# Kernel tuning notes

Hardware: AMD Instinct MI355X
Metric: run time of the kernel (lower is better)

Reference implementation:

```python
import jax, jax.numpy as jnp
import numpy as np

N, D_IN, D_HID, D_OUT = 100000, 128, 512, 256
EPS = 1e-5


def _kaiming_uniform(k, shape):
    # torch kaiming_uniform_(a=sqrt(5)) -> bound = sqrt(1/fan_in)
    fan_in = shape[1]
    bound = float(np.sqrt(1.0 / fan_in))
    return jax.random.uniform(k, shape, minval=-bound, maxval=bound, dtype=jnp.float32)


def setup_inputs() -> dict:
    key = jax.random.key(0)
    ks = jax.random.split(key, 10)
    in_set = jax.random.normal(ks[0], (N, D_IN), dtype=jnp.float32)
    matA0 = _kaiming_uniform(ks[1], (D_HID, D_IN))
    matB0 = _kaiming_uniform(ks[2], (D_HID, D_IN))
    matA1 = _kaiming_uniform(ks[3], (D_HID, D_HID))
    matB1 = _kaiming_uniform(ks[4], (D_HID, D_HID))
    matA2 = _kaiming_uniform(ks[5], (D_HID, D_HID))
    matB2 = _kaiming_uniform(ks[6], (D_HID, D_HID))
    ln_gamma = jnp.ones((D_HID,), dtype=jnp.float32)
    ln_beta = jnp.zeros((D_HID,), dtype=jnp.float32)
    out_bound = float(np.sqrt(1.0 / D_HID))
    out_w = jax.random.uniform(ks[7], (D_OUT, D_HID), minval=-out_bound, maxval=out_bound, dtype=jnp.float32)
    out_b = jax.random.uniform(ks[8], (D_OUT,), minval=-out_bound, maxval=out_bound, dtype=jnp.float32)
    return {"in_set": in_set, "matA0": matA0, "matB0": matB0, "matA1": matA1, "matB1": matB1,
            "matA2": matA2, "matB2": matB2, "ln_gamma": ln_gamma, "ln_beta": ln_beta,
            "out_w": out_w, "out_b": out_b}


def _layer(h, A, B, g, b):
    # f(x_i) = relu(LN(A x_i + B (sum_j x_j - x_i)))
    # vectorized: h @ (A-B)^T + total_sum @ B^T  (sum-minus-self identity)
    s = h.sum(axis=0)  # [d]
    h = h @ (A - B).T + s @ B.T  # [N, d_hid]
    mu = h.mean(axis=-1, keepdims=True)
    var = jnp.mean((h - mu) ** 2, axis=-1, keepdims=True)
    h = (h - mu) / jnp.sqrt(var + EPS) * g + b
    return jax.nn.relu(h)


def reference(in_set, matA0, matB0, matA1, matB1, matA2, matB2, ln_gamma, ln_beta, out_w, out_b):
    h = _layer(in_set, matA0, matB0, ln_gamma, ln_beta)
    h = _layer(h, matA1, matB1, ln_gamma, ln_beta)
    h = _layer(h, matA2, matB2, ln_gamma, ln_beta)
    h = h.max(axis=0)  # max-pool over set elements -> [d_hid]
    return h @ out_w.T + out_b  # [d_out]
```

## Files before the change

kernel.cpp:

```cpp
#include <hip/hip_runtime.h>
#include <hip/hip_bf16.h>

#define NPTS 100000
#define NPTS_PAD 100096
#define DHID 512
#define EPSV 1e-5f

typedef __attribute__((ext_vector_type(4))) float f32x4;

#define OFF_INBF   0UL
#define OFF_W0     12812288UL
#define OFF_W1     12877824UL
#define OFF_W2     13139968UL
#define OFF_C0     13402112UL
#define OFF_C1     13404160UL
#define OFF_C2     13406208UL
#define OFF_PARTS  13408256UL
#define OFF_PARTS2 16609280UL
#define OFF_PARTS3 16740352UL
#define OFF_H1     16756736UL
#define OFF_H2     68005888UL

typedef const __attribute__((address_space(1))) unsigned int* gp_t;
typedef __attribute__((address_space(3))) unsigned int* lp_t;

__device__ __forceinline__ void async_copy16(const void* g, void* l) {
    __builtin_amdgcn_global_load_lds((gp_t)g, (lp_t)l, 16, 0, 0);
}

__device__ __forceinline__ unsigned pack4_fp8(float a, float b, float c, float d) {
    unsigned v = (unsigned)__builtin_amdgcn_cvt_pk_fp8_f32(a, b, 0, false);
    v = (unsigned)__builtin_amdgcn_cvt_pk_fp8_f32(c, d, (int)v, true);
    return v;
}

__global__ __launch_bounds__(256) void cvt_pack_kernel(const float* __restrict__ in,
                                                       unsigned char* __restrict__ out) {
    long total = (long)NPTS * 2;
    long stride = (long)gridDim.x * blockDim.x;
    for (long idx = (long)blockIdx.x * blockDim.x + threadIdx.x; idx < total; idx += stride) {
        int kt = (int)(idx / NPTS);
        long r = idx - (long)kt * NPTS;
        const float* src = in + r * 128 + kt * 64;
        unsigned dw[16];
#pragma unroll
        for (int j = 0; j < 16; ++j)
            dw[j] = pack4_fp8(src[4 * j], src[4 * j + 1], src[4 * j + 2], src[4 * j + 3]);
        uint4* dst = (uint4*)(out + ((long)kt * NPTS_PAD + r) * 64);
#pragma unroll
        for (int j = 0; j < 4; ++j)
            dst[j] = make_uint4(dw[4 * j], dw[4 * j + 1], dw[4 * j + 2], dw[4 * j + 3]);
    }
}

__global__ __launch_bounds__(256) void wpack_all_kernel(const float* __restrict__ A0,
                                                        const float* __restrict__ B0,
                                                        const float* __restrict__ A1,
                                                        const float* __restrict__ B1,
                                                        const float* __restrict__ A2,
                                                        const float* __restrict__ B2,
                                                        unsigned long long* __restrict__ W0,
                                                        unsigned long long* __restrict__ W1,
                                                        unsigned long long* __restrict__ W2) {
    int idx = blockIdx.x * 256 + threadIdx.x;
    const float *A, *B; unsigned long long* W; int KD, u;
    if (idx < 8192)       { A = A0; B = B0; W = W0; KD = 128; u = idx; }
    else if (idx < 40960) { A = A1; B = B1; W = W1; KD = 512; u = idx - 8192; }
    else                  { A = A2; B = B2; W = W2; KD = 512; u = idx - 40960; if (u >= 32768) return; }
    int F = (KD / 64) * 8;
    int lane = u & 63;
    int f = (u >> 6) % F;
    int wid = u / (64 * F);
    int ks = f >> 3, fn = (f >> 1) & 3, s = f & 1;
    int row = wid * 64 + fn * 16 + (lane & 15);
    int kb = ks * 64 + s * 32 + (lane >> 4) * 8;
    const float* sa = A + (long)row * KD + kb;
    const float* sb = B + (long)row * KD + kb;
    unsigned lo = pack4_fp8(sa[0] - sb[0], sa[1] - sb[1], sa[2] - sb[2], sa[3] - sb[3]);
    unsigned hi = pack4_fp8(sa[4] - sb[4], sa[5] - sb[5], sa[6] - sb[6], sa[7] - sb[7]);
    W[u] = ((unsigned long long)hi << 32) | lo;
}

__global__ __launch_bounds__(256) void colsum_in_kernel(const float* __restrict__ in,
                                                        float* __restrict__ parts) {
    __shared__ float sh[256];
    int t = threadIdx.x, blk = blockIdx.x;
    int c = t & 127, half = t >> 7;
    long rbeg = (long)blk * 196 + half;
    long rend = (long)(blk + 1) * 196; if (rend > NPTS) rend = NPTS;
    float s = 0.f;
    for (long r = rbeg; r < rend; r += 2) s += in[r * 128 + c];
    sh[t] = s;
    __syncthreads();
    if (t < 128) parts[blk * 128 + t] = sh[t] + sh[t + 128];
}

__global__ void part_reduceW_kernel(const float* __restrict__ parts, int nparts, int width,
                                    int op, float* __restrict__ out) {
    int g = blockIdx.x, t = threadIdx.x;
    int chunk = (nparts + gridDim.x - 1) / gridDim.x;
    int b0 = g * chunk, b1 = b0 + chunk; if (b1 > nparts) b1 = nparts;
    float s = 0.f;
    for (int b = b0; b < b1; ++b) {
        float v = parts[(long)b * width + t];
        s = (op == 0) ? (s + v) : fmaxf(s, v);
    }
    out[(long)g * width + t] = s;
}

__global__ __launch_bounds__(64) void gemv_fold_kernel(const float* __restrict__ p3, int dsum,
                                                       const float* __restrict__ Bm,
                                                       const float* __restrict__ bias, int op,
                                                       float* __restrict__ out) {
    int j = blockIdx.x, t = threadIdx.x;
    float acc = 0.f;
    for (int d = t; d < dsum; d += 64) {
        float s = 0.f;
#pragma unroll
        for (int g = 0; g < 8; ++g) {
            float v = p3[(long)g * dsum + d];
            s = (op == 0) ? (s + v) : fmaxf(s, v);
        }
        acc += s * Bm[(long)j * dsum + d];
    }
#pragma unroll
    for (int m = 32; m >= 1; m >>= 1) acc += __shfl_down(acc, m);
    if (t == 0) out[j] = acc + (bias ? bias[j] : 0.0f);
}

template<int KD, bool STORE, int REDOP>
__global__ __launch_bounds__(512, 4)
void layer_kernel(const unsigned char* __restrict__ Xp, const unsigned long long* __restrict__ Wp,
                  const float* __restrict__ cvec, const float* __restrict__ gvec,
                  const float* __restrict__ bvec, unsigned char* __restrict__ Hout,
                  float* __restrict__ red_out) {
    static_assert(KD % 64 == 0, "");
    constexpr int NK = KD / 64;
    __shared__ __align__(128) char smem[NK * 4096];

    const int t = threadIdx.x;
    const int lane = t & 63;
    const int wid = t >> 6;
    const int ln15 = lane & 15;
    const int lg = lane >> 4;
    const long row0 = (long)blockIdx.x * 64;

    f32x4 acc[4][4];
#pragma unroll
    for (int i = 0; i < 4; ++i)
#pragma unroll
        for (int j = 0; j < 4; ++j) acc[i][j] = (f32x4){0.f, 0.f, 0.f, 0.f};

    if (t < 256) {
        const int sr = t >> 2;
        const int ss = t & 3;
        const char* Xsrc = (const char*)Xp + (row0 + sr) * 64 + ((ss ^ ((sr >> 1) & 3)) * 16);
#pragma unroll
        for (int kt = 0; kt < NK; ++kt)
            async_copy16(Xsrc + (long)kt * (NPTS_PAD * 64), smem + kt * 4096 + t * 16);
    }
    __syncthreads();

#define RD8X(BASE, r, sub) (*(const long*)((BASE) + (r) * 64 + \
        (((((sub) * 2 + (lg >> 1)) ^ (((r) >> 1) & 3)) * 16) + (lg & 1) * 8)))

    const unsigned long long* Wq = Wp + (long)wid * (NK * 8) * 64 + lane;
#pragma unroll
    for (int ks = 0; ks < NK; ++ks) {
        const char* Xs = smem + ks * 4096;
        long a0[4], a1[4];
#pragma unroll
        for (int fm = 0; fm < 4; ++fm) {
            int r = fm * 16 + ln15;
            a0[fm] = RD8X(Xs, r, 0);
            a1[fm] = RD8X(Xs, r, 1);
        }
#pragma unroll
        for (int fn = 0; fn < 4; ++fn) {
            long w0 = (long)Wq[(ks * 8 + fn * 2 + 0) * 64];
            long w1 = (long)Wq[(ks * 8 + fn * 2 + 1) * 64];
#pragma unroll
            for (int fm = 0; fm < 4; ++fm)
                acc[fm][fn] = __builtin_amdgcn_mfma_f32_16x16x32_fp8_fp8(a0[fm], w0, acc[fm][fn], 0, 0, 0);
#pragma unroll
            for (int fm = 0; fm < 4; ++fm)
                acc[fm][fn] = __builtin_amdgcn_mfma_f32_16x16x32_fp8_fp8(a1[fm], w1, acc[fm][fn], 0, 0, 0);
        }
    }
#undef RD8X
    __syncthreads();

    float* lnred_s = (float*)smem;
    float* lnred_q = (float*)(smem + 2048);
    float* lnmv    = (float*)(smem + 4096);

    const int cbase = wid * 64 + ln15;
    float cv[4], gv[4], bv[4];
#pragma unroll
    for (int fn = 0; fn < 4; ++fn) {
        int col = cbase + fn * 16;
        cv[fn] = cvec[col]; gv[fn] = gvec[col]; bv[fn] = bvec[col];
    }

#pragma unroll
    for (int fm = 0; fm < 4; ++fm)
#pragma unroll
        for (int fn = 0; fn < 4; ++fn) acc[fm][fn] += cv[fn];

    float rs[16], rq[16];
#pragma unroll
    for (int fm = 0; fm < 4; ++fm)
#pragma unroll
        for (int j = 0; j < 4; ++j) {
            float s = 0.f, q = 0.f;
#pragma unroll
            for (int fn = 0; fn < 4; ++fn) {
                float x = acc[fm][fn][j];
                s += x; q += x * x;
            }
            rs[fm * 4 + j] = s; rq[fm * 4 + j] = q;
        }
#pragma unroll
    for (int m = 1; m < 16; m <<= 1)
#pragma unroll
        for (int i = 0; i < 16; ++i) {
            rs[i] += __shfl_xor(rs[i], m);
            rq[i] += __shfl_xor(rq[i], m);
        }
    if (ln15 == 0) {
#pragma unroll
        for (int fm = 0; fm < 4; ++fm)
#pragma unroll
            for (int j = 0; j < 4; ++j) {
                int row = fm * 16 + lg * 4 + j;
                lnred_s[row * 8 + wid] = rs[fm * 4 + j];
                lnred_q[row * 8 + wid] = rq[fm * 4 + j];
            }
    }
    __syncthreads();
    if (t < 64) {
        float s = 0.f, q = 0.f;
#pragma unroll
        for (int w = 0; w < 8; ++w) { s += lnred_s[t * 8 + w]; q += lnred_q[t * 8 + w]; }
        float mu = s * (1.0f / 512.0f);
        float var = q * (1.0f / 512.0f) - mu * mu;
        lnmv[t * 2] = mu;
        lnmv[t * 2 + 1] = rsqrtf(var + EPSV);
    }
    __syncthreads();

#pragma unroll
    for (int fm = 0; fm < 4; ++fm)
#pragma unroll
        for (int j = 0; j < 4; ++j) {
            int rloc = fm * 16 + lg * 4 + j;
            long rglob = row0 + rloc;
            bool ok = rglob < NPTS;
            float mu = lnmv[rloc * 2], rstd = lnmv[rloc * 2 + 1];
#pragma unroll
            for (int fn = 0; fn < 4; ++fn) {
                float y = fmaxf((acc[fm][fn][j] - mu) * rstd * gv[fn] + bv[fn], 0.0f);
                acc[fm][fn][j] = ok ? y : 0.0f;
            }
            if (STORE && ok) {
#pragma unroll
                for (int p = 0; p < 2; ++p) {
                    unsigned u = (unsigned)__builtin_amdgcn_cvt_pk_fp8_f32(
                        acc[fm][2 * p][j], acc[fm][2 * p + 1][j], 0, false);
                    Hout[((long)wid * NPTS_PAD + rglob) * 64 + (2 * p) * 16 + ln15] =
                        (unsigned char)(u & 0xff);
                    Hout[((long)wid * NPTS_PAD + rglob) * 64 + (2 * p + 1) * 16 + ln15] =
                        (unsigned char)((u >> 8) & 0xff);
                }
            }
        }

    float cp[4];
#pragma unroll
    for (int fn = 0; fn < 4; ++fn) {
        float p = 0.f;
#pragma unroll
        for (int fm = 0; fm < 4; ++fm)
#pragma unroll
            for (int j = 0; j < 4; ++j) {
                float v = acc[fm][fn][j];
                p = (REDOP == 0) ? (p + v) : fmaxf(p, v);
            }
        cp[fn] = p;
    }
#pragma unroll
    for (int m = 16; m < 64; m <<= 1)
#pragma unroll
        for (int fn = 0; fn < 4; ++fn) {
            float o = __shfl_xor(cp[fn], m);
            cp[fn] = (REDOP == 0) ? (cp[fn] + o) : fmaxf(cp[fn], o);
        }
    if (lane < 16) {
#pragma unroll
        for (int fn = 0; fn < 4; ++fn)
            red_out[(long)blockIdx.x * 512 + wid * 64 + fn * 16 + lane] = cp[fn];
    }
}

extern "C" void kernel_launch(void* const* d_in, const int* in_sizes, int n_in,
                              void* d_out, int out_size, void* d_ws, size_t ws_size,
                              hipStream_t stream) {
    const float* in_set = (const float*)d_in[0];
    const float* A0 = (const float*)d_in[1];
    const float* B0 = (const float*)d_in[2];
    const float* A1 = (const float*)d_in[3];
    const float* B1 = (const float*)d_in[4];
    const float* A2 = (const float*)d_in[5];
    const float* B2 = (const float*)d_in[6];
    const float* ga = (const float*)d_in[7];
    const float* be = (const float*)d_in[8];
    const float* ow = (const float*)d_in[9];
    const float* ob = (const float*)d_in[10];
    float* outp = (float*)d_out;
    char* ws = (char*)d_ws;

    unsigned char* in_f8 = (unsigned char*)(ws + OFF_INBF);
    unsigned long long* W0p = (unsigned long long*)(ws + OFF_W0);
    unsigned long long* W1p = (unsigned long long*)(ws + OFF_W1);
    unsigned long long* W2p = (unsigned long long*)(ws + OFF_W2);
    float* c0 = (float*)(ws + OFF_C0);
    float* c1 = (float*)(ws + OFF_C1);
    float* c2 = (float*)(ws + OFF_C2);
    float* parts = (float*)(ws + OFF_PARTS);
    float* parts2 = (float*)(ws + OFF_PARTS2);
    float* parts3 = (float*)(ws + OFF_PARTS3);
    unsigned char* h1 = (unsigned char*)(ws + OFF_H1);
    unsigned char* h2 = (unsigned char*)(ws + OFF_H2);

    const int nblk = (NPTS + 63) / 64;

    cvt_pack_kernel<<<1024, 256, 0, stream>>>(in_set, in_f8);
    wpack_all_kernel<<<288, 256, 0, stream>>>(A0, B0, A1, B1, A2, B2, W0p, W1p, W2p);

    colsum_in_kernel<<<512, 256, 0, stream>>>(in_set, parts);
    part_reduceW_kernel<<<64, 128, 0, stream>>>(parts, 512, 128, 0, parts2);
    part_reduceW_kernel<<<8, 128, 0, stream>>>(parts2, 64, 128, 0, parts3);
    gemv_fold_kernel<<<512, 64, 0, stream>>>(parts3, 128, B0, nullptr, 0, c0);

    layer_kernel<128, true, 0><<<nblk, 512, 0, stream>>>(in_f8, W0p, c0, ga, be, h1, parts);
    part_reduceW_kernel<<<64, 512, 0, stream>>>(parts, nblk, 512, 0, parts2);
    part_reduceW_kernel<<<8, 512, 0, stream>>>(parts2, 64, 512, 0, parts3);
    gemv_fold_kernel<<<512, 64, 0, stream>>>(parts3, 512, B1, nullptr, 0, c1);

    layer_kernel<512, true, 0><<<nblk, 512, 0, stream>>>(h1, W1p, c1, ga, be, h2, parts);
    part_reduceW_kernel<<<64, 512, 0, stream>>>(parts, nblk, 512, 0, parts2);
    part_reduceW_kernel<<<8, 512, 0, stream>>>(parts2, 64, 512, 0, parts3);
    gemv_fold_kernel<<<512, 64, 0, stream>>>(parts3, 512, B2, nullptr, 0, c2);

    layer_kernel<512, false, 1><<<nblk, 512, 0, stream>>>(h2, W2p, c2, ga, be, nullptr, parts);
    part_reduceW_kernel<<<64, 512, 0, stream>>>(parts, nblk, 512, 1, parts2);
    part_reduceW_kernel<<<8, 512, 0, stream>>>(parts2, 64, 512, 1, parts3);
    gemv_fold_kernel<<<256, 64, 0, stream>>>(parts3, 512, ow, ob, 1, outp);
}
```

Measured before the change: 309.5 us.

## Interleave fp8 K layout so hidden activations store as packed dwords

Changes the fp8 packed layout of the K dimension so that element k=16*m+c sits at byte 4*c+m inside each 64-byte row chunk. The input packer, weight packer and epilogue store all switch to this permuted layout consistently. The epilogue now writes one 32-bit word per row instead of four scattered byte stores, which cuts store instruction count and partial-write traffic. The row-bound check is dropped from the store, so padded rows also get written, which is safe only because the buffer is padded.

```diff
diff --git a/kernel.cpp b/kernel.cpp
--- a/kernel.cpp
+++ b/kernel.cpp
@@ -44,8 +44,8 @@
         const float* src = in + r * 128 + kt * 64;
         unsigned dw[16];
 #pragma unroll
-        for (int j = 0; j < 16; ++j)
-            dw[j] = pack4_fp8(src[4 * j], src[4 * j + 1], src[4 * j + 2], src[4 * j + 3]);
+        for (int m = 0; m < 16; ++m)
+            dw[m] = pack4_fp8(src[m], src[16 + m], src[32 + m], src[48 + m]);
         uint4* dst = (uint4*)(out + ((long)kt * NPTS_PAD + r) * 64);
 #pragma unroll
         for (int j = 0; j < 4; ++j)
@@ -72,12 +72,15 @@
     int f = (u >> 6) % F;
     int wid = u / (64 * F);
     int ks = f >> 3, fn = (f >> 1) & 3, s = f & 1;
-    int row = wid * 64 + fn * 16 + (lane & 15);
-    int kb = ks * 64 + s * 32 + (lane >> 4) * 8;
-    const float* sa = A + (long)row * KD + kb;
-    const float* sb = B + (long)row * KD + kb;
-    unsigned lo = pack4_fp8(sa[0] - sb[0], sa[1] - sb[1], sa[2] - sb[2], sa[3] - sb[3]);
-    unsigned hi = pack4_fp8(sa[4] - sb[4], sa[5] - sb[5], sa[6] - sb[6], sa[7] - sb[7]);
+    int ln15 = lane & 15, lg = lane >> 4;
+    int row = wid * 64 + fn * 16 + ln15;
+    int c0 = s * 8 + lg * 2;
+    const float* sa = A + (long)row * KD + ks * 64;
+    const float* sb = B + (long)row * KD + ks * 64;
+    unsigned lo = pack4_fp8(sa[c0] - sb[c0], sa[16 + c0] - sb[16 + c0],
+                            sa[32 + c0] - sb[32 + c0], sa[48 + c0] - sb[48 + c0]);
+    unsigned hi = pack4_fp8(sa[c0 + 1] - sb[c0 + 1], sa[17 + c0] - sb[17 + c0],
+                            sa[33 + c0] - sb[33 + c0], sa[49 + c0] - sb[49 + c0]);
     W[u] = ((unsigned long long)hi << 32) | lo;
 }
 
@@ -262,16 +265,9 @@
                 float y = fmaxf((acc[fm][fn][j] - mu) * rstd * gv[fn] + bv[fn], 0.0f);
                 acc[fm][fn][j] = ok ? y : 0.0f;
             }
-            if (STORE && ok) {
-#pragma unroll
-                for (int p = 0; p < 2; ++p) {
-                    unsigned u = (unsigned)__builtin_amdgcn_cvt_pk_fp8_f32(
-                        acc[fm][2 * p][j], acc[fm][2 * p + 1][j], 0, false);
-                    Hout[((long)wid * NPTS_PAD + rglob) * 64 + (2 * p) * 16 + ln15] =
-                        (unsigned char)(u & 0xff);
-                    Hout[((long)wid * NPTS_PAD + rglob) * 64 + (2 * p + 1) * 16 + ln15] =
-                        (unsigned char)((u >> 8) & 0xff);
-                }
+            if (STORE) {
+                unsigned u = pack4_fp8(acc[fm][0][j], acc[fm][1][j], acc[fm][2][j], acc[fm][3][j]);
+                *(unsigned*)(Hout + ((long)wid * NPTS_PAD + rglob) * 64 + ln15 * 4) = u;
             }
         }
 
```

Measured after the change: 297.7 us. 3.8% less time.
